# Performance work log

Hardware: AMD Instinct MI355X
Metric: run time of the kernel (lower is better)

The kernel has to match this reference:

```python
import jax, jax.numpy as jnp
import numpy as np

N_MID = 100000
D = 64
B = 64
S = 256
K = 10
BIG_NEG = -2.0**32 + 1.0


def _din(q, facts, mask, W1, b1, W2, b2, W3, b3):
    # q broadcastable to facts shape; facts [..., T, D]; mask [..., T]
    qb = jnp.broadcast_to(q, facts.shape)
    x = jnp.concatenate([qb, facts, qb - facts, qb * facts], axis=-1)  # [..., T, 4D]
    h = jax.nn.sigmoid(x @ W1 + b1)
    h = jax.nn.sigmoid(h @ W2 + b2)
    s = (h @ W3 + b3)[..., 0]  # [..., T]
    s = jnp.where(mask == 1.0, s, BIG_NEG)
    a = jax.nn.softmax(s, axis=-1)
    return jnp.einsum('...t,...td->...d', a, facts)


def _prelu(x, alpha):
    return jnp.maximum(x, 0.0) + alpha * jnp.minimum(x, 0.0)


def setup_inputs():
    key = jax.random.key(0)
    ks = iter(jax.random.split(key, 48))
    def nrm(shape, scale=0.05):
        return jax.random.normal(next(ks), shape, dtype=jnp.float32) * scale
    inp = {}
    inp['mid'] = jax.random.randint(next(ks), (B,), 0, N_MID)
    inp['click_his'] = jax.random.randint(next(ks), (B, S), 0, N_MID)
    inp['unclick_his'] = jax.random.randint(next(ks), (B, K * S), 0, N_MID)
    inp['click_mask'] = jnp.ones((B, S), jnp.float32)
    inp['unclick_mask'] = jnp.ones((B, K * S), jnp.float32)
    inp['emb'] = nrm((N_MID, D), 0.1)
    for p in ('s', 'c', 'u'):  # search / click / unclick attention MLPs
        inp[p + 'W1'] = nrm((4 * D, 80)); inp[p + 'b1'] = jnp.zeros((80,), jnp.float32)
        inp[p + 'W2'] = nrm((80, 40));    inp[p + 'b2'] = jnp.zeros((40,), jnp.float32)
        inp[p + 'W3'] = nrm((40, 1));     inp[p + 'b3'] = jnp.zeros((1,), jnp.float32)
    F = 3 * D
    inp['bn_g'] = jnp.ones((F,), jnp.float32); inp['bn_b'] = jnp.zeros((F,), jnp.float32)
    inp['bn_m'] = jnp.zeros((F,), jnp.float32); inp['bn_v'] = jnp.ones((F,), jnp.float32)
    inp['fW1'] = nrm((F, 200)); inp['fb1'] = jnp.zeros((200,), jnp.float32); inp['a1'] = 0.25 * jnp.ones((200,), jnp.float32)
    inp['fW2'] = nrm((200, 80)); inp['fb2'] = jnp.zeros((80,), jnp.float32); inp['a2'] = 0.25 * jnp.ones((80,), jnp.float32)
    inp['fW3'] = nrm((80, 2)); inp['fb3'] = jnp.zeros((2,), jnp.float32)
    return inp


def reference(mid, click_his, unclick_his, click_mask, unclick_mask, emb,
              sW1, sb1, sW2, sb2, sW3, sb3,
              cW1, cb1, cW2, cb2, cW3, cb3,
              uW1, ub1, uW2, ub2, uW3, ub3,
              bn_g, bn_b, bn_m, bn_v,
              fW1, fb1, a1, fW2, fb2, a2, fW3, fb3):
    item = emb[mid]                                        # [B, D]
    click = emb[click_his] * click_mask[..., None]         # [B, S, D]
    unclick = emb[unclick_his] * unclick_mask[..., None]   # [B, K*S, D]
    uf = unclick.reshape(B, S, K, D)
    umask = unclick_mask.reshape(B, S, K)
    # din_attention_1: per clicked item, attend over its K unclicked items
    un_att = _din(click[:, :, None, :], uf, umask, sW1, sb1, sW2, sb2, sW3, sb3)  # [B, S, D]
    # denoise: project unclick rep onto click rep (shared component)
    dot = jnp.sum(un_att * click, axis=-1, keepdims=True)
    nrm2 = jnp.sum(click * click, axis=-1, keepdims=True) + 1e-12  # ||target||^2
    shared = dot * click / nrm2
    att1 = _din(item[:, None, :], click + shared, click_mask, cW1, cb1, cW2, cb2, cW3, cb3)  # [B, D]
    att2 = _din(item[:, None, :], un_att, click_mask, uW1, ub1, uW2, ub2, uW3, ub3)          # [B, D]
    x = jnp.concatenate([item, att1, att2], axis=-1)  # [B, 3D]
    x = (x - bn_m) / jnp.sqrt(bn_v + 1e-3) * bn_g + bn_b  # inference batchnorm
    x = _prelu(x @ fW1 + fb1, a1)
    x = _prelu(x @ fW2 + fb2, a2)
    logits = x @ fW3 + fb3
    return jax.nn.softmax(logits, axis=-1) + 1e-8
```

## Files before the change

### kernel.cpp

```cpp
#include <hip/hip_runtime.h>
#include <hip/hip_bf16.h>
#include <math.h>

#define BB 64
#define SS 256
#define KK 10
#define DD 64
#define FF 192
#define FH1 200
#define FH2 80
#define BIG_NEG_F (-4294967295.0f)

#define XSTR 200
#define H1STR 104

#define W1ELTS (80 * XSTR)
#define W2ELTS (48 * H1STR)
#define WREG   (W1ELTS + W2ELTS)

typedef __bf16 bfrag __attribute__((ext_vector_type(8)));
typedef float f32x4 __attribute__((ext_vector_type(4)));

__device__ __forceinline__ float sigm_(float x) { return 1.0f / (1.0f + __expf(-x)); }

__global__ __launch_bounds__(256) void k_prep(
    const float* __restrict__ sW1, const float* __restrict__ sW2,
    const float* __restrict__ cW1, const float* __restrict__ cW2,
    const float* __restrict__ uW1, const float* __restrict__ uW2,
    __bf16* __restrict__ Wt)
{
    const int p = blockIdx.x, g = blockIdx.y;
    const float* W1 = (p == 0) ? sW1 : (p == 1) ? cW1 : uW1;
    const float* W2 = (p == 0) ? sW2 : (p == 1) ? cW2 : uW2;
    __bf16* o1 = Wt + p * WREG;
    __bf16* o2 = o1 + W1ELTS;
    for (int e = g * 256 + threadIdx.x; e < 200 * 80; e += 2560) {
        const int k = e / 80, n = e % 80;
        float v;
        if (k < 64)       v = W1[k * 80 + n] + W1[(k + 128) * 80 + n];
        else if (k < 128) v = W1[k * 80 + n] - W1[(k + 64) * 80 + n];
        else if (k < 192) v = W1[(k + 64) * 80 + n];
        else              v = 0.0f;
        o1[n * XSTR + k] = (__bf16)v;
    }
    for (int e = g * 256 + threadIdx.x; e < W2ELTS; e += 2560) {
        const int n = e / H1STR, k = e % H1STR;
        o2[e] = (__bf16)((n < 40 && k < 80) ? W2[k * 40 + n] : 0.0f);
    }
}

__device__ __forceinline__ void mlp_core(
    const float* qv, const float* fv,
    const __bf16* __restrict__ sW1, __bf16* __restrict__ sH1w,
    const bfrag* wb2, const float* b1v, const float* b2v, const float* w3v,
    int quad, int l15, float* score)
{
    bfrag af[6];
    #pragma unroll
    for (int j = 0; j < 8; ++j) {
        af[0][j] = (__bf16)qv[j];
        af[1][j] = (__bf16)qv[8 + j];
        af[2][j] = (__bf16)fv[j];
        af[3][j] = (__bf16)fv[8 + j];
        af[4][j] = (__bf16)(qv[j] * fv[j]);
        af[5][j] = (__bf16)(qv[8 + j] * fv[8 + j]);
    }

    f32x4 acc[5];
    #pragma unroll
    for (int nt = 0; nt < 5; ++nt) acc[nt] = (f32x4){0.f, 0.f, 0.f, 0.f};
    {
        const __bf16* wbase = sW1 + l15 * XSTR + quad * 8;
        #pragma unroll
        for (int nt = 0; nt < 5; ++nt) {
            const __bf16* wp = wbase + nt * 16 * XSTR;
            #pragma unroll
            for (int kc = 0; kc < 6; ++kc)
                acc[nt] = __builtin_amdgcn_mfma_f32_16x16x32_bf16(
                    af[kc], *(const bfrag*)(wp + kc * 32), acc[nt], 0, 0, 0);
        }
    }

    #pragma unroll
    for (int nt = 0; nt < 5; ++nt) {
        #pragma unroll
        for (int rg = 0; rg < 4; ++rg)
            sH1w[(quad * 4 + rg) * H1STR + nt * 16 + l15] =
                (__bf16)sigm_(acc[nt][rg] + b1v[nt]);
    }
    #pragma unroll
    for (int rg = 0; rg < 4; ++rg)
        sH1w[(quad * 4 + rg) * H1STR + 80 + l15] = (__bf16)0.0f;

    bfrag af2[3];
    {
        const __bf16* hrow = sH1w + l15 * H1STR + quad * 8;
        #pragma unroll
        for (int kc = 0; kc < 3; ++kc) af2[kc] = *(const bfrag*)(hrow + kc * 32);
    }
    f32x4 acc2[3];
    #pragma unroll
    for (int nt = 0; nt < 3; ++nt) acc2[nt] = (f32x4){0.f, 0.f, 0.f, 0.f};
    #pragma unroll
    for (int nt = 0; nt < 3; ++nt)
        #pragma unroll
        for (int kc = 0; kc < 3; ++kc)
            acc2[nt] = __builtin_amdgcn_mfma_f32_16x16x32_bf16(
                af2[kc], wb2[nt * 3 + kc], acc2[nt], 0, 0, 0);

    float part[4] = {0.f, 0.f, 0.f, 0.f};
    #pragma unroll
    for (int nt = 0; nt < 3; ++nt) {
        #pragma unroll
        for (int rg = 0; rg < 4; ++rg)
            part[rg] += sigm_(acc2[nt][rg] + b2v[nt]) * w3v[nt];
    }
    #pragma unroll
    for (int off = 1; off < 16; off <<= 1) {
        #pragma unroll
        for (int rg = 0; rg < 4; ++rg)
            part[rg] += __shfl_xor(part[rg], off, 64);
    }
    #pragma unroll
    for (int rg = 0; rg < 4; ++rg) score[rg] = part[rg];
}

__global__ __launch_bounds__(256) void k_din0(
    const int* __restrict__ click_his, const int* __restrict__ unclick_his,
    const float* __restrict__ click_mask, const float* __restrict__ unclick_mask,
    const float* __restrict__ emb, const __bf16* __restrict__ Wt,
    const float* __restrict__ b1, const float* __restrict__ b2,
    const float* __restrict__ W3, const float* __restrict__ b3,
    float* __restrict__ unatt, float* __restrict__ coef)
{
    __shared__ __align__(16) __bf16 sW1[80 * XSTR];
    __shared__ __align__(16) __bf16 sH1[4][16 * H1STR];
    __shared__ float ssc[4][80];

    const int t = threadIdx.x;
    const int wave = t >> 6, lane = t & 63;
    const int quad = lane >> 4, l15 = lane & 15;

    {
        const uint4* s1 = (const uint4*)Wt;
        uint4* d1 = (uint4*)sW1;
        for (int e = t; e < W1ELTS / 8; e += 256) d1[e] = s1[e];
    }

    bfrag wb2[9];
    float b1v[5], b2v[3], w3v[3];
    {
        const __bf16* w2g = Wt + W1ELTS;
        #pragma unroll
        for (int nt = 0; nt < 3; ++nt)
            #pragma unroll
            for (int kc = 0; kc < 3; ++kc)
                wb2[nt * 3 + kc] = *(const bfrag*)(w2g + (nt * 16 + l15) * H1STR + kc * 32 + quad * 8);
        #pragma unroll
        for (int nt = 0; nt < 5; ++nt) b1v[nt] = b1[nt * 16 + l15];
        #pragma unroll
        for (int nt = 0; nt < 3; ++nt) {
            const int n = nt * 16 + l15;
            b2v[nt] = (n < 40) ? b2[n] : 0.0f;
            w3v[nt] = (n < 40) ? W3[n] : 0.0f;
        }
    }
    const float b3v = b3[0];

    const int wbase = (blockIdx.x * 4 + wave) * 80;
    const int c = quad * 8;

    auto gload = [&](int tt, float* qv, float* fv) {
        const int m  = wbase + tt * 16 + l15;
        const int bs = m / 10;
        const float* qp = emb + (size_t)click_his[bs] * DD;
        const float* fp = emb + (size_t)unclick_his[m] * DD;
        const float qs = click_mask[bs], fs = unclick_mask[m];
        *(float4*)(qv + 0)  = *(const float4*)(qp + c);
        *(float4*)(qv + 4)  = *(const float4*)(qp + c + 4);
        *(float4*)(qv + 8)  = *(const float4*)(qp + 32 + c);
        *(float4*)(qv + 12) = *(const float4*)(qp + 32 + c + 4);
        *(float4*)(fv + 0)  = *(const float4*)(fp + c);
        *(float4*)(fv + 4)  = *(const float4*)(fp + c + 4);
        *(float4*)(fv + 8)  = *(const float4*)(fp + 32 + c);
        *(float4*)(fv + 12) = *(const float4*)(fp + 32 + c + 4);
        #pragma unroll
        for (int i = 0; i < 16; ++i) { qv[i] *= qs; fv[i] *= fs; }
    };

    float qv[2][16], fv[2][16];
    gload(0, qv[0], fv[0]);
    __syncthreads();

    for (int tt = 0; tt < 5; ++tt) {
        if (tt < 4) gload(tt + 1, qv[(tt + 1) & 1], fv[(tt + 1) & 1]);
        float score[4];
        mlp_core(qv[tt & 1], fv[tt & 1], sW1, sH1[wave], wb2, b1v, b2v, w3v, quad, l15, score);
        if (l15 == 0) {
            #pragma unroll
            for (int rg = 0; rg < 4; ++rg) {
                const int r2 = tt * 16 + quad * 4 + rg;
                const int m2 = wbase + r2;
                ssc[wave][r2] = (unclick_mask[m2] == 1.0f) ? (score[rg] + b3v) : BIG_NEG_F;
            }
        }
    }
    __syncthreads();

    float fr[2][KK], qr[2];
    auto kload = [&](int j) {
        const int bsj = blockIdx.x * 32 + wave * 8 + j;
        const int jj = j & 1;
        #pragma unroll
        for (int k = 0; k < KK; ++k) {
            const int off = bsj * KK + k;
            fr[jj][k] = emb[(size_t)unclick_his[off] * DD + lane] * unclick_mask[off];
        }
        qr[jj] = emb[(size_t)click_his[bsj] * DD + lane] * click_mask[bsj];
    };
    kload(0);
    for (int j = 0; j < 8; ++j) {
        if (j < 7) kload(j + 1);
        const int bsj = blockIdx.x * 32 + wave * 8 + j;
        float a[KK];
        float mx = -INFINITY;
        #pragma unroll
        for (int k = 0; k < KK; ++k) { a[k] = ssc[wave][j * KK + k]; mx = fmaxf(mx, a[k]); }
        float sum = 0.0f;
        #pragma unroll
        for (int k = 0; k < KK; ++k) { a[k] = __expf(a[k] - mx); sum += a[k]; }
        const float inv = 1.0f / sum;
        float acc3 = 0.0f;
        #pragma unroll
        for (int k = 0; k < KK; ++k) acc3 += a[k] * fr[j & 1][k];
        acc3 *= inv;
        unatt[(size_t)bsj * DD + lane] = acc3;
        const float qv2 = qr[j & 1];
        float dp = acc3 * qv2, nq = qv2 * qv2;
        #pragma unroll
        for (int o = 32; o > 0; o >>= 1) {
            dp += __shfl_down(dp, o, 64);
            nq += __shfl_down(nq, o, 64);
        }
        if (lane == 0) coef[bsj] = 1.0f + dp / (nq + 1e-12f);
    }
}

__global__ __launch_bounds__(256) void k_din12(
    const int* __restrict__ mid, const int* __restrict__ click_his,
    const float* __restrict__ click_mask,
    const float* __restrict__ emb, const float* __restrict__ unatt,
    const float* __restrict__ coef, const __bf16* __restrict__ Wt,
    const float* __restrict__ cb1, const float* __restrict__ cb2,
    const float* __restrict__ cW3, const float* __restrict__ cb3,
    const float* __restrict__ ub1, const float* __restrict__ ub2,
    const float* __restrict__ uW3, const float* __restrict__ ub3,
    float* __restrict__ scores_c, float* __restrict__ scores_u)
{
    __shared__ __align__(16) __bf16 sW1[80 * XSTR];
    __shared__ __align__(16) __bf16 sH1[4][16 * H1STR];

    const int t = threadIdx.x;
    const int mode = blockIdx.y;
    const int wave = t >> 6, lane = t & 63;
    const int quad = lane >> 4, l15 = lane & 15;

    const float* b1 = mode ? ub1 : cb1;
    const float* b2 = mode ? ub2 : cb2;
    const float* W3 = mode ? uW3 : cW3;
    const float* b3 = mode ? ub3 : cb3;
    const __bf16* wreg = Wt + (mode + 1) * WREG;

    {
        const uint4* s1 = (const uint4*)wreg;
        uint4* d1 = (uint4*)sW1;
        for (int e = t; e < W1ELTS / 8; e += 256) d1[e] = s1[e];
    }

    bfrag wb2[9];
    float b1v[5], b2v[3], w3v[3];
    {
        const __bf16* w2g = wreg + W1ELTS;
        #pragma unroll
        for (int nt = 0; nt < 3; ++nt)
            #pragma unroll
            for (int kc = 0; kc < 3; ++kc)
                wb2[nt * 3 + kc] = *(const bfrag*)(w2g + (nt * 16 + l15) * H1STR + kc * 32 + quad * 8);
        #pragma unroll
        for (int nt = 0; nt < 5; ++nt) b1v[nt] = b1[nt * 16 + l15];
        #pragma unroll
        for (int nt = 0; nt < 3; ++nt) {
            const int n = nt * 16 + l15;
            b2v[nt] = (n < 40) ? b2[n] : 0.0f;
            w3v[nt] = (n < 40) ? W3[n] : 0.0f;
        }
    }
    const float b3v = b3[0];

    const int row = 16 * wave + l15;
    const int m   = blockIdx.x * 64 + row;
    const int b   = m >> 8;
    float qv[16], fv[16];
    {
        const float* qp = emb + (size_t)mid[b] * DD;
        const float* fp; float fs;
        if (mode == 0) { fp = emb + (size_t)click_his[m] * DD; fs = click_mask[m] * coef[m]; }
        else           { fp = unatt + (size_t)m * DD; fs = 1.0f; }
        const int c = quad * 8;
        *(float4*)(qv + 0)  = *(const float4*)(qp + c);
        *(float4*)(qv + 4)  = *(const float4*)(qp + c + 4);
        *(float4*)(qv + 8)  = *(const float4*)(qp + 32 + c);
        *(float4*)(qv + 12) = *(const float4*)(qp + 32 + c + 4);
        *(float4*)(fv + 0)  = *(const float4*)(fp + c);
        *(float4*)(fv + 4)  = *(const float4*)(fp + c + 4);
        *(float4*)(fv + 8)  = *(const float4*)(fp + 32 + c);
        *(float4*)(fv + 12) = *(const float4*)(fp + 32 + c + 4);
        #pragma unroll
        for (int i = 0; i < 16; ++i) fv[i] *= fs;
    }
    __syncthreads();

    float score[4];
    mlp_core(qv, fv, sW1, sH1[wave], wb2, b1v, b2v, w3v, quad, l15, score);

    if (l15 == 0) {
        float* dst = mode ? scores_u : scores_c;
        #pragma unroll
        for (int rg = 0; rg < 4; ++rg) {
            const int m2 = blockIdx.x * 64 + 16 * wave + quad * 4 + rg;
            dst[m2] = (click_mask[m2] == 1.0f) ? (score[rg] + b3v) : BIG_NEG_F;
        }
    }
}

__global__ __launch_bounds__(1024) void k_tail(
    const int* __restrict__ mid, const int* __restrict__ click_his,
    const float* __restrict__ click_mask,
    const float* __restrict__ emb, const float* __restrict__ unatt,
    const float* __restrict__ coef,
    const float* __restrict__ scores_c, const float* __restrict__ scores_u,
    const float* __restrict__ bn_g, const float* __restrict__ bn_b,
    const float* __restrict__ bn_m, const float* __restrict__ bn_v,
    const float* __restrict__ fW1, const float* __restrict__ fb1, const float* __restrict__ a1,
    const float* __restrict__ fW2, const float* __restrict__ fb2, const float* __restrict__ a2,
    const float* __restrict__ fW3, const float* __restrict__ fb3,
    float* __restrict__ out)
{
    const int b = blockIdx.x, t = threadIdx.x;
    const int wave = t >> 6, lane = t & 63;
    const int ty = wave >> 3, w8 = wave & 7;
    const int s0 = w8 * 32;

    __shared__ float sa[2][SS];
    __shared__ float smax[16], ssum[16];
    __shared__ float part[16][72];
    __shared__ float x[FF];
    __shared__ float ph1[4][FH1];
    __shared__ float h1s[FH1];
    __shared__ float ph2[8][FH2];
    __shared__ float h2s[FH2];
    __shared__ float red2[2];

    if (t < DD) x[t] = emb[(size_t)mid[b] * DD + t];

    const float* scp = ty ? scores_u : scores_c;
    const float sc = (lane < 32) ? scp[b * SS + s0 + lane] : -INFINITY;
    float mloc = sc;
    #pragma unroll
    for (int o = 32; o > 0; o >>= 1) mloc = fmaxf(mloc, __shfl_xor(mloc, o, 64));
    if (lane == 0) smax[wave] = mloc;
    __syncthreads();

    float mt = smax[ty * 8];
    #pragma unroll
    for (int i = 1; i < 8; ++i) mt = fmaxf(mt, smax[ty * 8 + i]);
    const float e = (lane < 32) ? __expf(sc - mt) : 0.0f;
    if (lane < 32) sa[ty][s0 + lane] = e;
    float sloc = e;
    #pragma unroll
    for (int o = 32; o > 0; o >>= 1) sloc += __shfl_xor(sloc, o, 64);
    if (lane == 0) ssum[wave] = sloc;
    __syncthreads();

    float den = 0.0f;
    #pragma unroll
    for (int i = 0; i < 8; ++i) den += ssum[ty * 8 + i];
    const float inv = 1.0f / den;

    float acc = 0.0f;
    #pragma unroll 8
    for (int i = 0; i < 32; ++i) {
        const int s2 = s0 + i;
        const int bs = b * SS + s2;
        const float fv = ty ? unatt[(size_t)bs * DD + lane]
                            : emb[(size_t)click_his[bs] * DD + lane] * click_mask[bs] * coef[bs];
        acc += sa[ty][s2] * fv;
    }
    part[wave][lane] = acc * inv;
    __syncthreads();

    if (t < 128) {
        const int tt = t >> 6, d = t & 63;
        float v = 0.0f;
        #pragma unroll
        for (int i = 0; i < 8; ++i) v += part[tt * 8 + i][d];
        x[DD + tt * DD + d] = v;
    }
    __syncthreads();

    if (t < FF) x[t] = (x[t] - bn_m[t]) * rsqrtf(bn_v[t] + 1e-3f) * bn_g[t] + bn_b[t];
    __syncthreads();

    if (t < 800) {
        const int n = t % FH1, cc = t / FH1;
        float p = 0.0f;
        #pragma unroll 8
        for (int i = cc * 48; i < cc * 48 + 48; ++i) p += x[i] * fW1[i * FH1 + n];
        ph1[cc][n] = p;
    }
    __syncthreads();
    if (t < FH1) {
        const float a = ph1[0][t] + ph1[1][t] + ph1[2][t] + ph1[3][t] + fb1[t];
        h1s[t] = fmaxf(a, 0.0f) + a1[t] * fminf(a, 0.0f);
    }
    __syncthreads();

    if (t < 640) {
        const int n = t % FH2, cc = t / FH2;
        float p = 0.0f;
        #pragma unroll 5
        for (int i = cc * 25; i < cc * 25 + 25; ++i) p += h1s[i] * fW2[i * FH2 + n];
        ph2[cc][n] = p;
    }
    __syncthreads();
    if (t < FH2) {
        float a = fb2[t];
        #pragma unroll
        for (int cc = 0; cc < 8; ++cc) a += ph2[cc][t];
        h2s[t] = fmaxf(a, 0.0f) + a2[t] * fminf(a, 0.0f);
    }
    __syncthreads();

    if (t < 128) {
        const int o = t >> 6;
        float p = h2s[lane] * fW3[lane * 2 + o];
        if (lane < 16) p += h2s[64 + lane] * fW3[(64 + lane) * 2 + o];
        #pragma unroll
        for (int off = 32; off > 0; off >>= 1) p += __shfl_down(p, off, 64);
        if (lane == 0) red2[o] = p + fb3[o];
    }
    __syncthreads();
    if (t == 0) {
        const float l0 = red2[0], l1 = red2[1];
        const float mx = fmaxf(l0, l1);
        const float e0 = __expf(l0 - mx), e1 = __expf(l1 - mx);
        const float invs = 1.0f / (e0 + e1);
        out[b * 2 + 0] = e0 * invs + 1e-8f;
        out[b * 2 + 1] = e1 * invs + 1e-8f;
    }
}

extern "C" void kernel_launch(void* const* d_in, const int* in_sizes, int n_in,
                              void* d_out, int out_size, void* d_ws, size_t ws_size,
                              hipStream_t stream) {
    const int*   mid          = (const int*)d_in[0];
    const int*   click_his    = (const int*)d_in[1];
    const int*   unclick_his  = (const int*)d_in[2];
    const float* click_mask   = (const float*)d_in[3];
    const float* unclick_mask = (const float*)d_in[4];
    const float* emb          = (const float*)d_in[5];
    const float* sW1 = (const float*)d_in[6];  const float* sb1 = (const float*)d_in[7];
    const float* sW2 = (const float*)d_in[8];  const float* sb2 = (const float*)d_in[9];
    const float* sW3 = (const float*)d_in[10]; const float* sb3 = (const float*)d_in[11];
    const float* cW1 = (const float*)d_in[12]; const float* cb1 = (const float*)d_in[13];
    const float* cW2 = (const float*)d_in[14]; const float* cb2 = (const float*)d_in[15];
    const float* cW3 = (const float*)d_in[16]; const float* cb3 = (const float*)d_in[17];
    const float* uW1 = (const float*)d_in[18]; const float* ub1 = (const float*)d_in[19];
    const float* uW2 = (const float*)d_in[20]; const float* ub2 = (const float*)d_in[21];
    const float* uW3 = (const float*)d_in[22]; const float* ub3 = (const float*)d_in[23];
    const float* bn_g = (const float*)d_in[24]; const float* bn_b = (const float*)d_in[25];
    const float* bn_m = (const float*)d_in[26]; const float* bn_v = (const float*)d_in[27];
    const float* fW1 = (const float*)d_in[28]; const float* fb1 = (const float*)d_in[29];
    const float* a1  = (const float*)d_in[30];
    const float* fW2 = (const float*)d_in[31]; const float* fb2 = (const float*)d_in[32];
    const float* a2  = (const float*)d_in[33];
    const float* fW3 = (const float*)d_in[34]; const float* fb3 = (const float*)d_in[35];

    float* out = (float*)d_out;

    char* w = (char*)d_ws;
    __bf16* Wt      = (__bf16*)(w + 0);
    float* scores_c = (float*)(w + 125952);
    float* scores_u = (float*)(w + 191488);
    float* coef     = (float*)(w + 257024);
    float* unatt    = (float*)(w + 322560);

    hipLaunchKernelGGL(k_prep, dim3(3, 10), dim3(256), 0, stream,
        sW1, sW2, cW1, cW2, uW1, uW2, Wt);

    hipLaunchKernelGGL(k_din0, dim3(512), dim3(256), 0, stream,
        click_his, unclick_his, click_mask, unclick_mask, emb, Wt,
        sb1, sb2, sW3, sb3, unatt, coef);

    hipLaunchKernelGGL(k_din12, dim3(256, 2), dim3(256), 0, stream,
        mid, click_his, click_mask, emb, unatt, coef, Wt,
        cb1, cb2, cW3, cb3, ub1, ub2, uW3, ub3, scores_c, scores_u);

    hipLaunchKernelGGL(k_tail, dim3(BB), dim3(1024), 0, stream,
        mid, click_his, click_mask, emb, unatt, coef, scores_c, scores_u,
        bn_g, bn_b, bn_m, bn_v, fW1, fb1, a1, fW2, fb2, a2, fW3, fb3, out);
}
```

Before: 261.0 us.

## Drop register double-buffering in din0, halve din12 grid, widen prep grid

Removes the software-pipelined prefetch buffers in k_din0 (both the MLP gather and the K-softmax phase), so each iteration loads inline with unroll disabled. This lowers register pressure and may raise occupancy. The cost is losing explicit load/compute overlap. k_din12 now has each wave process two 16-row tiles, which halves the grid and amortises the per-block weight staging. k_prep uses four times as many blocks so the weight transform runs with more parallelism.

```diff
diff --git a/kernel.cpp b/kernel.cpp
--- a/kernel.cpp
+++ b/kernel.cpp
@@ -34,7 +34,7 @@
     const float* W2 = (p == 0) ? sW2 : (p == 1) ? cW2 : uW2;
     __bf16* o1 = Wt + p * WREG;
     __bf16* o2 = o1 + W1ELTS;
-    for (int e = g * 256 + threadIdx.x; e < 200 * 80; e += 2560) {
+    for (int e = g * 256 + threadIdx.x; e < 200 * 80; e += 10240) {
         const int k = e / 80, n = e % 80;
         float v;
         if (k < 64)       v = W1[k * 80 + n] + W1[(k + 128) * 80 + n];
@@ -43,7 +43,7 @@
         else              v = 0.0f;
         o1[n * XSTR + k] = (__bf16)v;
     }
-    for (int e = g * 256 + threadIdx.x; e < W2ELTS; e += 2560) {
+    for (int e = g * 256 + threadIdx.x; e < W2ELTS; e += 10240) {
         const int n = e / H1STR, k = e % H1STR;
         o2[e] = (__bf16)((n < 40 && k < 80) ? W2[k * 40 + n] : 0.0f);
     }
@@ -169,33 +169,30 @@
 
     const int wbase = (blockIdx.x * 4 + wave) * 80;
     const int c = quad * 8;
-
-    auto gload = [&](int tt, float* qv, float* fv) {
-        const int m  = wbase + tt * 16 + l15;
-        const int bs = m / 10;
-        const float* qp = emb + (size_t)click_his[bs] * DD;
-        const float* fp = emb + (size_t)unclick_his[m] * DD;
-        const float qs = click_mask[bs], fs = unclick_mask[m];
-        *(float4*)(qv + 0)  = *(const float4*)(qp + c);
-        *(float4*)(qv + 4)  = *(const float4*)(qp + c + 4);
-        *(float4*)(qv + 8)  = *(const float4*)(qp + 32 + c);
-        *(float4*)(qv + 12) = *(const float4*)(qp + 32 + c + 4);
-        *(float4*)(fv + 0)  = *(const float4*)(fp + c);
-        *(float4*)(fv + 4)  = *(const float4*)(fp + c + 4);
-        *(float4*)(fv + 8)  = *(const float4*)(fp + 32 + c);
-        *(float4*)(fv + 12) = *(const float4*)(fp + 32 + c + 4);
-        #pragma unroll
-        for (int i = 0; i < 16; ++i) { qv[i] *= qs; fv[i] *= fs; }
-    };
-
-    float qv[2][16], fv[2][16];
-    gload(0, qv[0], fv[0]);
-    __syncthreads();
-
+    __syncthreads();
+
+    #pragma unroll 1
     for (int tt = 0; tt < 5; ++tt) {
-        if (tt < 4) gload(tt + 1, qv[(tt + 1) & 1], fv[(tt + 1) & 1]);
+        float qv[16], fv[16];
+        {
+            const int m  = wbase + tt * 16 + l15;
+            const int bs = m / 10;
+            const float* qp = emb + (size_t)click_his[bs] * DD;
+            const float* fp = emb + (size_t)unclick_his[m] * DD;
+            const float qs = click_mask[bs], fs = unclick_mask[m];
+            *(float4*)(qv + 0)  = *(const float4*)(qp + c);
+            *(float4*)(qv + 4)  = *(const float4*)(qp + c + 4);
+            *(float4*)(qv + 8)  = *(const float4*)(qp + 32 + c);
+            *(float4*)(qv + 12) = *(const float4*)(qp + 32 + c + 4);
+            *(float4*)(fv + 0)  = *(const float4*)(fp + c);
+            *(float4*)(fv + 4)  = *(const float4*)(fp + c + 4);
+            *(float4*)(fv + 8)  = *(const float4*)(fp + 32 + c);
+            *(float4*)(fv + 12) = *(const float4*)(fp + 32 + c + 4);
+            #pragma unroll
+            for (int i = 0; i < 16; ++i) { qv[i] *= qs; fv[i] *= fs; }
+        }
         float score[4];
-        mlp_core(qv[tt & 1], fv[tt & 1], sW1, sH1[wave], wb2, b1v, b2v, w3v, quad, l15, score);
+        mlp_core(qv, fv, sW1, sH1[wave], wb2, b1v, b2v, w3v, quad, l15, score);
         if (l15 == 0) {
             #pragma unroll
             for (int rg = 0; rg < 4; ++rg) {
@@ -205,22 +202,9 @@
             }
         }
     }
-    __syncthreads();
-
-    float fr[2][KK], qr[2];
-    auto kload = [&](int j) {
-        const int bsj = blockIdx.x * 32 + wave * 8 + j;
-        const int jj = j & 1;
-        #pragma unroll
-        for (int k = 0; k < KK; ++k) {
-            const int off = bsj * KK + k;
-            fr[jj][k] = emb[(size_t)unclick_his[off] * DD + lane] * unclick_mask[off];
-        }
-        qr[jj] = emb[(size_t)click_his[bsj] * DD + lane] * click_mask[bsj];
-    };
-    kload(0);
+
+    #pragma unroll 1
     for (int j = 0; j < 8; ++j) {
-        if (j < 7) kload(j + 1);
         const int bsj = blockIdx.x * 32 + wave * 8 + j;
         float a[KK];
         float mx = -INFINITY;
@@ -232,10 +216,13 @@
         const float inv = 1.0f / sum;
         float acc3 = 0.0f;
         #pragma unroll
-        for (int k = 0; k < KK; ++k) acc3 += a[k] * fr[j & 1][k];
+        for (int k = 0; k < KK; ++k) {
+            const int off = bsj * KK + k;
+            acc3 += a[k] * (emb[(size_t)unclick_his[off] * DD + lane] * unclick_mask[off]);
+        }
         acc3 *= inv;
         unatt[(size_t)bsj * DD + lane] = acc3;
-        const float qv2 = qr[j & 1];
+        const float qv2 = emb[(size_t)click_his[bsj] * DD + lane] * click_mask[bsj];
         float dp = acc3 * qv2, nq = qv2 * qv2;
         #pragma unroll
         for (int o = 32; o > 0; o >>= 1) {
@@ -296,39 +283,40 @@
         }
     }
     const float b3v = b3[0];
-
-    const int row = 16 * wave + l15;
-    const int m   = blockIdx.x * 64 + row;
-    const int b   = m >> 8;
-    float qv[16], fv[16];
-    {
-        const float* qp = emb + (size_t)mid[b] * DD;
-        const float* fp; float fs;
-        if (mode == 0) { fp = emb + (size_t)click_his[m] * DD; fs = click_mask[m] * coef[m]; }
-        else           { fp = unatt + (size_t)m * DD; fs = 1.0f; }
-        const int c = quad * 8;
-        *(float4*)(qv + 0)  = *(const float4*)(qp + c);
-        *(float4*)(qv + 4)  = *(const float4*)(qp + c + 4);
-        *(float4*)(qv + 8)  = *(const float4*)(qp + 32 + c);
-        *(float4*)(qv + 12) = *(const float4*)(qp + 32 + c + 4);
-        *(float4*)(fv + 0)  = *(const float4*)(fp + c);
-        *(float4*)(fv + 4)  = *(const float4*)(fp + c + 4);
-        *(float4*)(fv + 8)  = *(const float4*)(fp + 32 + c);
-        *(float4*)(fv + 12) = *(const float4*)(fp + 32 + c + 4);
-        #pragma unroll
-        for (int i = 0; i < 16; ++i) fv[i] *= fs;
-    }
-    __syncthreads();
-
-    float score[4];
-    mlp_core(qv, fv, sW1, sH1[wave], wb2, b1v, b2v, w3v, quad, l15, score);
-
-    if (l15 == 0) {
-        float* dst = mode ? scores_u : scores_c;
-        #pragma unroll
-        for (int rg = 0; rg < 4; ++rg) {
-            const int m2 = blockIdx.x * 64 + 16 * wave + quad * 4 + rg;
-            dst[m2] = (click_mask[m2] == 1.0f) ? (score[rg] + b3v) : BIG_NEG_F;
+    const int c = quad * 8;
+    __syncthreads();
+
+    #pragma unroll 1
+    for (int tt = 0; tt < 2; ++tt) {
+        const int row = wave * 32 + tt * 16 + l15;
+        const int m   = blockIdx.x * 128 + row;
+        const int b   = m >> 8;
+        float qv[16], fv[16];
+        {
+            const float* qp = emb + (size_t)mid[b] * DD;
+            const float* fp; float fs;
+            if (mode == 0) { fp = emb + (size_t)click_his[m] * DD; fs = click_mask[m] * coef[m]; }
+            else           { fp = unatt + (size_t)m * DD; fs = 1.0f; }
+            *(float4*)(qv + 0)  = *(const float4*)(qp + c);
+            *(float4*)(qv + 4)  = *(const float4*)(qp + c + 4);
+            *(float4*)(qv + 8)  = *(const float4*)(qp + 32 + c);
+            *(float4*)(qv + 12) = *(const float4*)(qp + 32 + c + 4);
+            *(float4*)(fv + 0)  = *(const float4*)(fp + c);
+            *(float4*)(fv + 4)  = *(const float4*)(fp + c + 4);
+            *(float4*)(fv + 8)  = *(const float4*)(fp + 32 + c);
+            *(float4*)(fv + 12) = *(const float4*)(fp + 32 + c + 4);
+            #pragma unroll
+            for (int i = 0; i < 16; ++i) fv[i] *= fs;
+        }
+        float score[4];
+        mlp_core(qv, fv, sW1, sH1[wave], wb2, b1v, b2v, w3v, quad, l15, score);
+        if (l15 == 0) {
+            float* dst = mode ? scores_u : scores_c;
+            #pragma unroll
+            for (int rg = 0; rg < 4; ++rg) {
+                const int m2 = blockIdx.x * 128 + wave * 32 + tt * 16 + quad * 4 + rg;
+                dst[m2] = (click_mask[m2] == 1.0f) ? (score[rg] + b3v) : BIG_NEG_F;
+            }
         }
     }
 }
@@ -495,14 +483,14 @@
     float* coef     = (float*)(w + 257024);
     float* unatt    = (float*)(w + 322560);
 
-    hipLaunchKernelGGL(k_prep, dim3(3, 10), dim3(256), 0, stream,
+    hipLaunchKernelGGL(k_prep, dim3(3, 40), dim3(256), 0, stream,
         sW1, sW2, cW1, cW2, uW1, uW2, Wt);
 
     hipLaunchKernelGGL(k_din0, dim3(512), dim3(256), 0, stream,
         click_his, unclick_his, click_mask, unclick_mask, emb, Wt,
         sb1, sb2, sW3, sb3, unatt, coef);
 
-    hipLaunchKernelGGL(k_din12, dim3(256, 2), dim3(256), 0, stream,
+    hipLaunchKernelGGL(k_din12, dim3(128, 2), dim3(256), 0, stream,
         mid, click_his, click_mask, emb, unatt, coef, Wt,
         cb1, cb2, cW3, cb3, ub1, ub2, uW3, ub3, scores_c, scores_u);
 
```

Measured after the change: 225.1 us. 1.16x faster.
